# Kernel tuning notes

Measured on AMD Instinct MI355X. Metric: run time of the kernel, lower is better.

Reference implementation:

```python
import jax, jax.numpy as jnp
import numpy as np

B, S, D, H, DFF = 2, 2048, 1024, 16, 4096
DH = D // H
EPS = 1e-12


def _layer_norm(x, g, b):
    mu = jnp.mean(x, axis=-1, keepdims=True)
    var = jnp.mean(jnp.square(x - mu), axis=-1, keepdims=True)
    return (x - mu) * jax.lax.rsqrt(var + EPS) * g + b


def setup_inputs() -> dict:
    key = jax.random.key(0)
    ks = jax.random.split(key, 12)
    s = 0.02
    return {
        "query": jax.random.normal(ks[0], (B, S, D), jnp.float32),
        "key_in": jax.random.normal(ks[1], (B, S, D), jnp.float32),
        "value_in": jax.random.normal(ks[2], (B, S, D), jnp.float32),
        "attention_mask": jnp.zeros((B, 1, 1, S), jnp.float32),
        # weights stored [in, out] (i.e., torch Linear weight transposed)
        "Wq": jax.random.normal(ks[3], (D, D), jnp.float32) * s,
        "bq": jnp.zeros((D,), jnp.float32),
        "Wk": jax.random.normal(ks[4], (D, D), jnp.float32) * s,
        "bk": jnp.zeros((D,), jnp.float32),
        "Wv": jax.random.normal(ks[5], (D, D), jnp.float32) * s,
        "bv": jnp.zeros((D,), jnp.float32),
        "Wo": jax.random.normal(ks[6], (D, D), jnp.float32) * s,
        "bo": jnp.zeros((D,), jnp.float32),
        "ln1_g": jnp.ones((D,), jnp.float32),
        "ln1_b": jnp.zeros((D,), jnp.float32),
        "Wi": jax.random.normal(ks[7], (D, DFF), jnp.float32) * s,
        "bi": jnp.zeros((DFF,), jnp.float32),
        "Wd": jax.random.normal(ks[8], (DFF, D), jnp.float32) * s,
        "bd": jnp.zeros((D,), jnp.float32),
        "ln2_g": jnp.ones((D,), jnp.float32),
        "ln2_b": jnp.zeros((D,), jnp.float32),
    }


def reference(query, key_in, value_in, attention_mask, Wq, bq, Wk, bk, Wv, bv,
              Wo, bo, ln1_g, ln1_b, Wi, bi, Wd, bd, ln2_g, ln2_b):
    # projections -> [B, H, S, DH]
    q = (query @ Wq + bq).reshape(B, S, H, DH).transpose(0, 2, 1, 3)
    k = (key_in @ Wk + bk).reshape(B, S, H, DH).transpose(0, 2, 1, 3)
    v = (value_in @ Wv + bv).reshape(B, S, H, DH).transpose(0, 2, 1, 3)
    # eager attention: full [B,H,S,S] score matrix, as in the source
    scores = jnp.einsum("bhqd,bhkd->bhqk", q, k) / jnp.sqrt(jnp.float32(DH))
    scores = scores + attention_mask
    probs = jax.nn.softmax(scores, axis=-1)  # dropout p=0 -> identity
    ctx = jnp.einsum("bhqk,bhkd->bhqd", probs, v)
    ctx = ctx.transpose(0, 2, 1, 3).reshape(B, S, D)
    attn_out = ctx @ Wo + bo
    attn_out = _layer_norm(attn_out + query, ln1_g, ln1_b)
    inter = jax.nn.gelu(attn_out @ Wi + bi, approximate=False)
    layer_out = inter @ Wd + bd
    return _layer_norm(layer_out + attn_out, ln2_g, ln2_b)
```

## Files before the change

### kernel.cpp

```cpp
#include <hip/hip_runtime.h>
#include <hip/hip_bf16.h>
#include <cmath>

#define B_   2
#define S_   2048
#define D_   1024
#define H_   16
#define DFF_ 4096
#define DH_  64
#define M_   (B_*S_)

typedef __bf16 bfx8 __attribute__((ext_vector_type(8)));
typedef __bf16 bfx4 __attribute__((ext_vector_type(4)));
typedef float  fx4  __attribute__((ext_vector_type(4)));

__device__ __forceinline__ float fast_exp2(float x) {
  float r;
  asm volatile("v_exp_f32 %0, %1" : "=v"(r) : "v"(x));
  return r;
}

__device__ __forceinline__ float fast_erf(float x) {
  float ax = fabsf(x);
  float t  = __builtin_amdgcn_rcpf(fmaf(0.3275911f, ax, 1.0f));
  float p  = fmaf(1.061405429f, t, -1.453152027f);
  p = fmaf(p, t, 1.421413741f);
  p = fmaf(p, t, -0.284496736f);
  p = fmaf(p, t, 0.254829592f);
  p = p * t;
  float e  = fast_exp2(-ax * ax * 1.44269504f);
  float r  = 1.0f - p * e;
  return copysignf(r, x);
}

__device__ __forceinline__ void gload_lds16(const void* g, void* l) {
  __builtin_amdgcn_global_load_lds((__attribute__((address_space(1))) void*)(g),
                                   (__attribute__((address_space(3))) void*)(l),
                                   16, 0, 0);
}

struct CvtArgs { const float* in[3]; __bf16* out[3]; };

__global__ __launch_bounds__(256)
void to_bf16_3_kernel(CvtArgs args, int n) {
  int z = blockIdx.y;
  int i = (blockIdx.x * 256 + threadIdx.x) * 4;
  if (i < n) {
    float4 v = *(const float4*)(args.in[z] + i);
    bfx4 o;
    o[0] = (__bf16)v.x; o[1] = (__bf16)v.y; o[2] = (__bf16)v.z; o[3] = (__bf16)v.w;
    *(bfx4*)(args.out[z] + i) = o;
  }
}

__global__ __launch_bounds__(256)
void scale_mask_kernel(const float* __restrict__ in, float* __restrict__ out, int n) {
  int i = blockIdx.x * 256 + threadIdx.x;
  if (i < n) out[i] = in[i] * 1.44269504f;
}

struct TrArgs { const float* in[6]; __bf16* out[6]; };

__global__ __launch_bounds__(256)
void transpose_all_kernel(TrArgs a) {
  __shared__ float t[32][33];
  int bid = blockIdx.x;
  int wsel, tr, tc, R, C;
  if (bid < 4096) {
    wsel = bid >> 10; int l = bid & 1023;
    tr = l >> 5; tc = l & 31; R = D_; C = D_;
  } else if (bid < 8192) {
    wsel = 4; int l = bid - 4096;
    tr = l >> 7; tc = l & 127; R = D_; C = DFF_;
  } else {
    wsel = 5; int l = bid - 8192;
    tr = l >> 5; tc = l & 31; R = DFF_; C = D_;
  }
  const float* in = a.in[wsel];
  __bf16* out = a.out[wsel];
  int r0 = tr * 32, c0 = tc * 32;
  int tx = threadIdx.x & 31, ty = threadIdx.x >> 5;
#pragma unroll
  for (int j = 0; j < 4; ++j) {
    int r = ty + j * 8;
    t[r][tx] = in[(size_t)(r0 + r) * C + c0 + tx];
  }
  __syncthreads();
#pragma unroll
  for (int j = 0; j < 4; ++j) {
    int c = ty + j * 8;
    out[(size_t)(c0 + c) * R + r0 + tx] = (__bf16)t[tx][c];
  }
}

__global__ __launch_bounds__(256)
void transpose_v_kernel(const __bf16* __restrict__ vb, __bf16* __restrict__ vt) {
  __shared__ __bf16 t[32][33];
  int bh = blockIdx.z;
  int b = bh >> 4, h = bh & 15;
  int s0 = blockIdx.x * 32, d0 = blockIdx.y * 32;
  int tx = threadIdx.x, ty = threadIdx.y;
#pragma unroll
  for (int j = 0; j < 4; ++j) {
    int s = ty + j * 8;
    t[s][tx] = vb[(size_t)((b * S_ + s0 + s) * H_ + h) * DH_ + d0 + tx];
  }
  __syncthreads();
#pragma unroll
  for (int j = 0; j < 4; ++j) {
    int d = ty + j * 8;
    vt[(size_t)(bh * DH_ + d0 + d) * S_ + s0 + tx] = t[tx][d];
  }
}

template<int MODE, int TBN>
__global__ __launch_bounds__(256)
void gemm_kernel(const __bf16* __restrict__ A, const __bf16* __restrict__ Bt,
                 const float* __restrict__ bias, const void* __restrict__ res,
                 void* __restrict__ out, int Ndim, int Kdim) {
  __shared__ alignas(16) __bf16 As[2 * 128 * 64];
  __shared__ alignas(16) __bf16 Bs[2 * TBN * 64];
  const int tid  = threadIdx.x;
  const int lane = tid & 63;
  const int w    = tid >> 6;
  const int wm   = w >> 1, wn = w & 1;
  constexpr int NF = TBN / 32;
  const int m0 = blockIdx.y * 128, n0 = blockIdx.x * TBN;

  fx4 acc[4][NF];
#pragma unroll
  for (int i = 0; i < 4; ++i)
#pragma unroll
    for (int j = 0; j < NF; ++j) acc[i][j] = {0.f, 0.f, 0.f, 0.f};

  const int KT = Kdim / 64;

  auto stage = [&](int kt, int buf) {
    const int kb0 = kt * 64;
#pragma unroll
    for (int i = 0; i < 4; ++i) {
      int o   = tid * 16 + i * 4096;
      int row = o >> 7, cb = o & 127;
      int cbs = cb ^ ((row & 7) << 4);
      gload_lds16((const char*)A + ((size_t)(m0 + row) * Kdim + kb0) * 2 + cbs,
                  (char*)As + buf * 16384 + o);
    }
#pragma unroll
    for (int i = 0; i < NF; ++i) {
      int o   = tid * 16 + i * 4096;
      int row = o >> 7, cb = o & 127;
      int cbs = cb ^ ((row & 7) << 4);
      gload_lds16((const char*)Bt + ((size_t)(n0 + row) * Kdim + kb0) * 2 + cbs,
                  (char*)Bs + buf * (TBN * 128) + o);
    }
  };

  stage(0, 0);
  asm volatile("s_waitcnt vmcnt(0)" ::: "memory");
  __builtin_amdgcn_s_barrier();
  __builtin_amdgcn_sched_barrier(0);

  for (int kt = 0; kt < KT; ++kt) {
    if (kt + 1 < KT) stage(kt + 1, (kt + 1) & 1);
    __builtin_amdgcn_sched_barrier(0);
    if (kt > 0) {
      if (kt + 1 < KT) {
        if constexpr (TBN == 64) asm volatile("s_waitcnt vmcnt(6)" ::: "memory");
        else                     asm volatile("s_waitcnt vmcnt(8)" ::: "memory");
      } else {
        asm volatile("s_waitcnt vmcnt(0)" ::: "memory");
      }
      __builtin_amdgcn_s_barrier();
      __builtin_amdgcn_sched_barrier(0);
    }
    const char* Ab = (const char*)As + (kt & 1) * 16384;
    const char* Bb = (const char*)Bs + (kt & 1) * (TBN * 128);

#pragma unroll
    for (int kk = 0; kk < 2; ++kk) {
      bfx8 afr[4], bfr[NF];
      const int cb = kk * 64 + ((lane >> 4) << 4);
#pragma unroll
      for (int mf = 0; mf < 4; ++mf) {
        int row = wm * 64 + mf * 16 + (lane & 15);
        afr[mf] = *(const bfx8*)(Ab + row * 128 + (cb ^ ((row & 7) << 4)));
      }
#pragma unroll
      for (int nf = 0; nf < NF; ++nf) {
        int row = wn * (TBN / 2) + nf * 16 + (lane & 15);
        bfr[nf] = *(const bfx8*)(Bb + row * 128 + (cb ^ ((row & 7) << 4)));
      }
#pragma unroll
      for (int mf = 0; mf < 4; ++mf)
#pragma unroll
        for (int nf = 0; nf < NF; ++nf)
          acc[mf][nf] = __builtin_amdgcn_mfma_f32_16x16x32_bf16(afr[mf], bfr[nf],
                                                                acc[mf][nf], 0, 0, 0);
    }
    __builtin_amdgcn_s_barrier();
    __builtin_amdgcn_sched_barrier(0);
  }

#pragma unroll
  for (int mf = 0; mf < 4; ++mf) {
#pragma unroll
    for (int nf = 0; nf < NF; ++nf) {
      int col = n0 + wn * (TBN / 2) + nf * 16 + (lane & 15);
      float bvl = bias[col];
#pragma unroll
      for (int r = 0; r < 4; ++r) {
        int rowg = m0 + wm * 64 + mf * 16 + ((lane >> 4) << 2) + r;
        float v = acc[mf][nf][r] + bvl;
        if (MODE == 2) v = 0.5f * v * (1.0f + fast_erf(v * 0.70710678118654752f));
        if (MODE == 4) v += (float)((const __bf16*)res)[(size_t)rowg * Ndim + col];
        if (MODE == 1) ((float*)out)[(size_t)rowg * Ndim + col] = v;
        else           ((__bf16*)out)[(size_t)rowg * Ndim + col] = (__bf16)v;
      }
    }
  }
}

__device__ __forceinline__ void stage_a256(const __bf16* __restrict__ A, int m0,
                                           int Kdim, int tile, int h, char* Asm) {
  char* dst = Asm + (tile & 1) * 32768;
  const int kb0 = tile * 64;
  const int tid = threadIdx.x;
#pragma unroll
  for (int it = 0; it < 2; ++it) {
    int o = tid * 16 + it * 8192;
    int lrow = o >> 7, cb = o & 127;
    int r = (lrow & 63) + h * 64 + ((lrow >> 6) << 7);
    int csrc = cb ^ ((r & 7) << 4);
    gload_lds16((const char*)A + ((size_t)(m0 + r) * Kdim + kb0) * 2 + csrc,
                dst + r * 128 + cb);
  }
}
__device__ __forceinline__ void stage_b256(const __bf16* __restrict__ Bt, int n0,
                                           int Kdim, int tile, int h, char* Bsm) {
  char* dst = Bsm + (tile & 1) * 32768;
  const int kb0 = tile * 64;
  const int tid = threadIdx.x;
#pragma unroll
  for (int it = 0; it < 2; ++it) {
    int o = tid * 16 + it * 8192;
    int lrow = o >> 7, cb = o & 127;
    int r = h * 128 + lrow;
    int csrc = cb ^ ((r & 7) << 4);
    gload_lds16((const char*)Bt + ((size_t)(n0 + r) * Kdim + kb0) * 2 + csrc,
                dst + r * 128 + cb);
  }
}

template<int MODE>
__device__ __forceinline__ void gemm256_body(const __bf16* __restrict__ A,
                                             const __bf16* __restrict__ Bt,
                                             const float* __restrict__ bias,
                                             void* __restrict__ out,
                                             int Ndim, int Kdim, int m0, int n0) {
  extern __shared__ char smem[];
  char* Asm = smem;
  char* Bsm = smem + 65536;
  const int tid  = threadIdx.x;
  const int lane = tid & 63;
  const int w    = tid >> 6;
  const int wm   = w >> 2;
  const int wn   = w & 3;
  const int g    = lane >> 4;
  const int ql   = lane & 15;
  const int KT   = Kdim / 64;

  fx4 acc[8][4];
#pragma unroll
  for (int i = 0; i < 8; ++i)
#pragma unroll
    for (int j = 0; j < 4; ++j) acc[i][j] = {0.f, 0.f, 0.f, 0.f};

  stage_a256(A, m0, Kdim, 0, 0, Asm);
  stage_a256(A, m0, Kdim, 0, 1, Asm);
  stage_b256(Bt, n0, Kdim, 0, 0, Bsm);
  stage_b256(Bt, n0, Kdim, 0, 1, Bsm);
  stage_a256(A, m0, Kdim, 1, 0, Asm);
  asm volatile("s_waitcnt vmcnt(2)" ::: "memory");
  __builtin_amdgcn_s_barrier();
  __builtin_amdgcn_sched_barrier(0);

  for (int t = 0; t < KT; ++t) {
    const char* Ab = Asm + (t & 1) * 32768;
    const char* Bb = Bsm + (t & 1) * 32768;
#pragma unroll
    for (int p = 0; p < 4; ++p) {
      const int ah = p >> 1, kk = p & 1;
      if (p == 0 && t + 1 < KT) stage_a256(A, m0, Kdim, t + 1, 1, Asm);
      if (p == 1 && t + 1 < KT) stage_b256(Bt, n0, Kdim, t + 1, 0, Bsm);
      if (p == 2 && t + 1 < KT) stage_b256(Bt, n0, Kdim, t + 1, 1, Bsm);
      if (p == 3 && t + 2 < KT) stage_a256(A, m0, Kdim, t + 2, 0, Asm);
      __builtin_amdgcn_sched_barrier(0);

      bfx8 af[4], bf[4];
      const int cbv = kk * 64 + g * 16;
#pragma unroll
      for (int j = 0; j < 4; ++j) {
        int arow = wm * 128 + (ah * 4 + j) * 16 + ql;
        af[j] = *(const bfx8*)(Ab + arow * 128 + (cbv ^ ((arow & 7) << 4)));
      }
#pragma unroll
      for (int nf = 0; nf < 4; ++nf) {
        int brow = wn * 64 + nf * 16 + ql;
        bf[nf] = *(const bfx8*)(Bb + brow * 128 + (cbv ^ ((brow & 7) << 4)));
      }
      __builtin_amdgcn_sched_barrier(0);
      __builtin_amdgcn_s_barrier();
      asm volatile("s_waitcnt lgkmcnt(0)" ::: "memory");
      __builtin_amdgcn_sched_barrier(0);
      __builtin_amdgcn_s_setprio(1);
#pragma unroll
      for (int j = 0; j < 4; ++j)
#pragma unroll
        for (int nf = 0; nf < 4; ++nf)
          acc[ah * 4 + j][nf] = __builtin_amdgcn_mfma_f32_16x16x32_bf16(
              af[j], bf[nf], acc[ah * 4 + j][nf], 0, 0, 0);
      __builtin_amdgcn_s_setprio(0);
      __builtin_amdgcn_s_barrier();
      __builtin_amdgcn_sched_barrier(0);
    }
    if (t + 1 < KT) {
      if (t + 2 < KT) asm volatile("s_waitcnt vmcnt(2)" ::: "memory");
      else            asm volatile("s_waitcnt vmcnt(0)" ::: "memory");
      __builtin_amdgcn_s_barrier();
      __builtin_amdgcn_sched_barrier(0);
    }
  }

#pragma unroll
  for (int mf = 0; mf < 8; ++mf) {
#pragma unroll
    for (int nf = 0; nf < 4; ++nf) {
      int col = n0 + wn * 64 + nf * 16 + ql;
      float bvl = bias[col];
#pragma unroll
      for (int r = 0; r < 4; ++r) {
        int rowg = m0 + wm * 128 + mf * 16 + g * 4 + r;
        float v = acc[mf][nf][r] + bvl;
        if (MODE == 2) v = 0.5f * v * (1.0f + fast_erf(v * 0.70710678118654752f));
        if (MODE == 1) ((float*)out)[(size_t)rowg * Ndim + col] = v;
        else          ((__bf16*)out)[(size_t)rowg * Ndim + col] = (__bf16)v;
      }
    }
  }
}

template<int MODE>
__global__ __launch_bounds__(512)
void gemm256_kernel(const __bf16* __restrict__ A, const __bf16* __restrict__ Bt,
                    const float* __restrict__ bias, void* __restrict__ out,
                    int Ndim, int Kdim) {
  gemm256_body<MODE>(A, Bt, bias, out, Ndim, Kdim,
                     blockIdx.y * 256, blockIdx.x * 256);
}

struct QKVArgs {
  const __bf16* A[3]; const __bf16* Bt[3]; const float* bias[3]; __bf16* out[3];
};

__global__ __launch_bounds__(512)
void qkv256_kernel(QKVArgs args, int Ndim, int Kdim) {
  int z = blockIdx.z;
  gemm256_body<0>(args.A[z], args.Bt[z], args.bias[z], (void*)args.out[z],
                  Ndim, Kdim, blockIdx.y * 256, blockIdx.x * 256);
}

__global__ __launch_bounds__(512)
void attn_kernel(const __bf16* __restrict__ Qb, const __bf16* __restrict__ Kb,
                 const __bf16* __restrict__ Vt, const float* __restrict__ mask2,
                 __bf16* __restrict__ ctx) {
  __shared__ alignas(16) __bf16 Ks[3 * 64 * 64];
  __shared__ alignas(16) __bf16 Vs[3 * 64 * 64];
  __shared__ alignas(16) __bf16 Ps[8 * 16 * 64];
  __shared__ alignas(16) float  Ms[2048];

  const int tid  = threadIdx.x;
  const int lane = tid & 63;
  const int w    = tid >> 6;
  const int g    = lane >> 4;
  const int ql   = lane & 15;
  const int bh   = blockIdx.y;
  const int b    = bh >> 4;
  const int h    = bh & 15;
  const int q0   = blockIdx.x * 128;

  const size_t kbase  = ((size_t)(b * S_)) * D_ + h * DH_;
  const size_t vtbase = (size_t)bh * DH_ * S_;
  const int NT = S_ / 64;

  char* Qsm = (char*)Ps;
  const size_t qbase = ((size_t)(b * S_) + q0) * D_ + h * DH_;
#pragma unroll
  for (int i = 0; i < 2; ++i) {
    int o   = tid * 16 + i * 8192;
    int row = o >> 7, cb = o & 127;
    int cbs = cb ^ ((row & 7) << 4);
    gload_lds16((const char*)Qb + (qbase + (size_t)row * D_) * 2 + cbs, Qsm + o);
  }
  {
    int o = tid * 16;
    gload_lds16((const char*)mask2 + (size_t)b * S_ * 4 + o, (char*)Ms + o);
  }
  {
    int o   = tid * 16;
    int row = o >> 7, cb = o & 127;
    int cbs = cb ^ ((row & 7) << 4);
    gload_lds16((const char*)Kb + (kbase + (size_t)row * D_) * 2 + cbs, (char*)Ks + o);
    gload_lds16((const char*)Vt + (vtbase + (size_t)row * S_) * 2 + cbs, (char*)Vs + o);
    gload_lds16((const char*)Kb + (kbase + (size_t)(64 + row) * D_) * 2 + cbs,
                (char*)Ks + 8192 + o);
    gload_lds16((const char*)Vt + (vtbase + (size_t)row * S_ + 64) * 2 + cbs,
                (char*)Vs + 8192 + o);
  }
  asm volatile("s_waitcnt vmcnt(4)" ::: "memory");
  __builtin_amdgcn_s_barrier();
  __builtin_amdgcn_sched_barrier(0);

  bfx8 aq[2];
  {
    int row = w * 16 + ql;
#pragma unroll
    for (int kk = 0; kk < 2; ++kk) {
      int cb = kk * 64 + g * 16;
      aq[kk] = *(const bfx8*)(Qsm + row * 128 + (cb ^ ((row & 7) << 4)));
    }
  }
  __syncthreads();
  asm volatile("s_waitcnt vmcnt(2)" ::: "memory");
  __builtin_amdgcn_s_barrier();
  __builtin_amdgcn_sched_barrier(0);

  float mrun = -1e30f, lrun = 0.f;
  fx4 acc[4];
#pragma unroll
  for (int d = 0; d < 4; ++d) acc[d] = {0.f, 0.f, 0.f, 0.f};

  char* pw = (char*)Ps + w * 2048;
  const float SCL = 0.18033688f;

  for (int t = 0; t < NT; ++t) {
    const int kv0 = t * 64;
    if (t + 2 < NT) {
      int o   = tid * 16;
      int row = o >> 7, cb = o & 127;
      int cbs = cb ^ ((row & 7) << 4);
      int nkv = kv0 + 128;
      int bo  = ((t + 2) % 3) * 8192;
      gload_lds16((const char*)Kb + (kbase + (size_t)(nkv + row) * D_) * 2 + cbs,
                  (char*)Ks + bo + o);
      gload_lds16((const char*)Vt + (vtbase + (size_t)row * S_ + nkv) * 2 + cbs,
                  (char*)Vs + bo + o);
    }
    __builtin_amdgcn_sched_barrier(0);
    if (t > 0) {
      if (t + 2 < NT)      asm volatile("s_waitcnt vmcnt(4)" ::: "memory");
      else if (t + 1 < NT) asm volatile("s_waitcnt vmcnt(2)" ::: "memory");
      else                 asm volatile("s_waitcnt vmcnt(0)" ::: "memory");
      __builtin_amdgcn_s_barrier();
      __builtin_amdgcn_sched_barrier(0);
    }
    const char* Kc = (const char*)Ks + (t % 3) * 8192;
    const char* Vc = (const char*)Vs + (t % 3) * 8192;

    fx4 sc[4];
#pragma unroll
    for (int nf = 0; nf < 4; ++nf) sc[nf] = {0.f, 0.f, 0.f, 0.f};
#pragma unroll
    for (int kk = 0; kk < 2; ++kk) {
      const int cb = kk * 64 + g * 16;
      bfx8 bk[4];
#pragma unroll
      for (int nf = 0; nf < 4; ++nf) {
        int row = nf * 16 + ql;
        bk[nf] = *(const bfx8*)(Kc + row * 128 + (cb ^ ((row & 7) << 4)));
      }
#pragma unroll
      for (int nf = 0; nf < 4; ++nf)
        sc[nf] = __builtin_amdgcn_mfma_f32_16x16x32_bf16(bk[nf], aq[kk], sc[nf], 0, 0, 0);
    }

    float sv[4][4];
#pragma unroll
    for (int nf = 0; nf < 4; ++nf) {
      float4 mk = *(const float4*)((const char*)Ms + (kv0 + nf * 16 + g * 4) * 4);
      sv[nf][0] = sc[nf][0] * SCL + mk.x;
      sv[nf][1] = sc[nf][1] * SCL + mk.y;
      sv[nf][2] = sc[nf][2] * SCL + mk.z;
      sv[nf][3] = sc[nf][3] * SCL + mk.w;
    }
    float t0 = fmaxf(fmaxf(sv[0][0], sv[0][1]), fmaxf(sv[0][2], sv[0][3]));
    float t1 = fmaxf(fmaxf(sv[1][0], sv[1][1]), fmaxf(sv[1][2], sv[1][3]));
    float t2 = fmaxf(fmaxf(sv[2][0], sv[2][1]), fmaxf(sv[2][2], sv[2][3]));
    float t3 = fmaxf(fmaxf(sv[3][0], sv[3][1]), fmaxf(sv[3][2], sv[3][3]));
    float mx = fmaxf(fmaxf(t0, t1), fmaxf(t2, t3));
    mx = fmaxf(mx, __shfl_xor(mx, 16));
    mx = fmaxf(mx, __shfl_xor(mx, 32));

    if (!__all(mx <= mrun + 8.0f)) {
      float mnew  = fmaxf(mrun, mx);
      float alpha = fast_exp2(mrun - mnew);
      lrun *= alpha;
      float af[4];
#pragma unroll
      for (int r = 0; r < 4; ++r) af[r] = __shfl(alpha, g * 4 + r);
#pragma unroll
      for (int d = 0; d < 4; ++d)
#pragma unroll
        for (int r = 0; r < 4; ++r) acc[d][r] *= af[r];
      mrun = mnew;
    }

    float ps[4];
#pragma unroll
    for (int nf = 0; nf < 4; ++nf) {
#pragma unroll
      for (int r = 0; r < 4; ++r) sv[nf][r] = fast_exp2(sv[nf][r] - mrun);
      ps[nf] = (sv[nf][0] + sv[nf][1]) + (sv[nf][2] + sv[nf][3]);
    }
    float rs = (ps[0] + ps[1]) + (ps[2] + ps[3]);
    rs += __shfl_xor(rs, 16);
    rs += __shfl_xor(rs, 32);
    lrun += rs;

#pragma unroll
    for (int nf = 0; nf < 4; ++nf) {
      bfx4 pv;
      pv[0] = (__bf16)sv[nf][0]; pv[1] = (__bf16)sv[nf][1];
      pv[2] = (__bf16)sv[nf][2]; pv[3] = (__bf16)sv[nf][3];
      int c = (nf * 32 + g * 8) ^ ((ql & 7) << 4);
      *(bfx4*)(pw + ql * 128 + c) = pv;
    }

    asm volatile("s_waitcnt lgkmcnt(0)" ::: "memory");
    __builtin_amdgcn_sched_barrier(0);

#pragma unroll
    for (int kk = 0; kk < 2; ++kk) {
      int prow = ql;
      int cb   = kk * 64 + g * 16;
      bfx8 ap  = *(const bfx8*)((const char*)pw + prow * 128 + (cb ^ ((prow & 7) << 4)));
#pragma unroll
      for (int d = 0; d < 4; ++d) {
        int vrow = d * 16 + ql;
        bfx8 bv  = *(const bfx8*)(Vc + vrow * 128 + (cb ^ ((vrow & 7) << 4)));
        acc[d] = __builtin_amdgcn_mfma_f32_16x16x32_bf16(ap, bv, acc[d], 0, 0, 0);
      }
    }

    __builtin_amdgcn_s_barrier();
    __builtin_amdgcn_sched_barrier(0);
  }

  float linv = 1.0f / lrun;
#pragma unroll
  for (int r = 0; r < 4; ++r) {
    float inv = __shfl(linv, g * 4 + r);
    int qrow = q0 + w * 16 + g * 4 + r;
    size_t base = ((size_t)(b * S_) + qrow) * D_ + h * DH_;
#pragma unroll
    for (int d = 0; d < 4; ++d)
      ctx[base + d * 16 + ql] = (__bf16)(acc[d][r] * inv);
  }
}

template<bool WRITE_BF16>
__global__ __launch_bounds__(256)
void ln_kernel(const __bf16* __restrict__ a,
               const float* __restrict__ g, const float* __restrict__ beta,
               float* __restrict__ outf, __bf16* __restrict__ outb) {
  const int row = blockIdx.x;
  const int tid = threadIdx.x;
  const size_t base = (size_t)row * D_;
  bfx4 xa = *(const bfx4*)(a + base + tid * 4);
  float x[4] = {(float)xa[0], (float)xa[1], (float)xa[2], (float)xa[3]};
  float s = x[0] + x[1] + x[2] + x[3];
#pragma unroll
  for (int m = 1; m < 64; m <<= 1) s += __shfl_xor(s, m);
  __shared__ float red[8];
  if ((tid & 63) == 0) red[tid >> 6] = s;
  __syncthreads();
  float mu = (red[0] + red[1] + red[2] + red[3]) * (1.0f / D_);
  float v0 = 0.f;
#pragma unroll
  for (int i = 0; i < 4; ++i) { float d = x[i] - mu; v0 += d * d; }
#pragma unroll
  for (int m = 1; m < 64; m <<= 1) v0 += __shfl_xor(v0, m);
  if ((tid & 63) == 0) red[4 + (tid >> 6)] = v0;
  __syncthreads();
  float var = (red[4] + red[5] + red[6] + red[7]) * (1.0f / D_);
  float rs = rsqrtf(var + 1e-12f);
#pragma unroll
  for (int i = 0; i < 4; ++i) {
    int col = tid * 4 + i;
    x[i] = (x[i] - mu) * rs * g[col] + beta[col];
  }
  if (WRITE_BF16) {
    bfx4 o;
    o[0] = (__bf16)x[0]; o[1] = (__bf16)x[1]; o[2] = (__bf16)x[2]; o[3] = (__bf16)x[3];
    *(bfx4*)(outb + base + tid * 4) = o;
  } else {
    *(float4*)(outf + base + tid * 4) = make_float4(x[0], x[1], x[2], x[3]);
  }
}

extern "C" void kernel_launch(void* const* d_in, const int* in_sizes, int n_in,
                              void* d_out, int out_size, void* d_ws, size_t ws_size,
                              hipStream_t stream) {
  const float* query    = (const float*)d_in[0];
  const float* key_in   = (const float*)d_in[1];
  const float* value_in = (const float*)d_in[2];
  const float* mask     = (const float*)d_in[3];
  const float* Wq = (const float*)d_in[4];  const float* bq = (const float*)d_in[5];
  const float* Wk = (const float*)d_in[6];  const float* bk = (const float*)d_in[7];
  const float* Wv = (const float*)d_in[8];  const float* bv = (const float*)d_in[9];
  const float* Wo = (const float*)d_in[10]; const float* bo = (const float*)d_in[11];
  const float* ln1g = (const float*)d_in[12]; const float* ln1b = (const float*)d_in[13];
  const float* Wi = (const float*)d_in[14]; const float* bi = (const float*)d_in[15];
  const float* Wd = (const float*)d_in[16]; const float* bd = (const float*)d_in[17];
  const float* ln2g = (const float*)d_in[18]; const float* ln2b = (const float*)d_in[19];

  char* ws = (char*)d_ws;
  const size_t MB = 1ull << 20;
  if (ws_size < 112 * MB) return;

  __bf16* xq   = (__bf16*)(ws + 0 * MB);
  __bf16* xk   = (__bf16*)(ws + 8 * MB);
  float*  mask2= (float*)(ws + 8 * MB);
  __bf16* xv   = (__bf16*)(ws + 16 * MB);
  __bf16* x1b  = (__bf16*)(ws + 16 * MB);
  __bf16* qb   = (__bf16*)(ws + 24 * MB);
  __bf16* inter= (__bf16*)(ws + 24 * MB);
  __bf16* kb   = (__bf16*)(ws + 32 * MB);
  __bf16* vb   = (__bf16*)(ws + 40 * MB);
  __bf16* alinb= (__bf16*)(ws + 40 * MB);
  __bf16* vt   = (__bf16*)(ws + 48 * MB);
  __bf16* ctxb = (__bf16*)(ws + 56 * MB);
  __bf16* ffb  = (__bf16*)(ws + 56 * MB);
  __bf16* wqt  = (__bf16*)(ws + 88 * MB);
  __bf16* wkt  = (__bf16*)(ws + 90 * MB);
  __bf16* wvt  = (__bf16*)(ws + 92 * MB);
  __bf16* wot  = (__bf16*)(ws + 94 * MB);
  __bf16* wit  = (__bf16*)(ws + 96 * MB);
  __bf16* wdt  = (__bf16*)(ws + 104 * MB);

  dim3 b256(256);
  dim3 tblk(32, 8);
  const int n1 = M_ * D_;

  CvtArgs ca;
  ca.in[0] = query; ca.in[1] = key_in; ca.in[2] = value_in;
  ca.out[0] = xq;   ca.out[1] = xk;    ca.out[2] = xv;
  to_bf16_3_kernel<<<dim3(n1 / 1024, 3), b256, 0, stream>>>(ca, n1);

  TrArgs ta;
  ta.in[0] = Wq; ta.in[1] = Wk; ta.in[2] = Wv; ta.in[3] = Wo; ta.in[4] = Wi; ta.in[5] = Wd;
  ta.out[0] = wqt; ta.out[1] = wkt; ta.out[2] = wvt; ta.out[3] = wot;
  ta.out[4] = wit; ta.out[5] = wdt;
  transpose_all_kernel<<<dim3(12288), b256, 0, stream>>>(ta);

  QKVArgs qa;
  qa.A[0] = xq;  qa.A[1] = xk;  qa.A[2] = xv;
  qa.Bt[0] = wqt; qa.Bt[1] = wkt; qa.Bt[2] = wvt;
  qa.bias[0] = bq; qa.bias[1] = bk; qa.bias[2] = bv;
  qa.out[0] = qb; qa.out[1] = kb; qa.out[2] = vb;
  qkv256_kernel<<<dim3(D_ / 256, M_ / 256, 3), dim3(512), 131072, stream>>>(qa, D_, D_);

  transpose_v_kernel<<<dim3(S_ / 32, 2, B_ * H_), tblk, 0, stream>>>(vb, vt);

  scale_mask_kernel<<<dim3((B_ * S_ + 255) / 256), b256, 0, stream>>>(mask, mask2, B_ * S_);

  attn_kernel<<<dim3(S_ / 128, B_ * H_), dim3(512), 0, stream>>>(qb, kb, vt, mask2, ctxb);

  gemm_kernel<4, 64><<<dim3(D_ / 64, M_ / 128), b256, 0, stream>>>(ctxb, wot, bo, xq, (void*)alinb, D_, D_);

  ln_kernel<true><<<dim3(M_), b256, 0, stream>>>(alinb, ln1g, ln1b, nullptr, x1b);

  gemm256_kernel<2><<<dim3(DFF_ / 256, M_ / 256), dim3(512), 131072, stream>>>(x1b, wit, bi, (void*)inter, DFF_, D_);

  gemm_kernel<4, 64><<<dim3(D_ / 64, M_ / 128), b256, 0, stream>>>(inter, wdt, bd, x1b, (void*)ffb, D_, DFF_);

  ln_kernel<false><<<dim3(M_), b256, 0, stream>>>(ffb, ln2g, ln2b, (float*)d_out, nullptr);
}
```

Baseline: 257.3 us.

## Merge prep kernels, fold mask scaling into attention, compute row sums via MFMA

Merges the weight-transpose and input bf16-conversion kernels into one launch, and removes the separate mask-scaling kernel by scaling the mask in LDS inside the attention kernel. The softmax row sum is now accumulated with an extra MFMA against a ones vector instead of VALU adds and cross-lane shuffles. s_setprio hints are added around MFMA blocks. These changes cut launch overhead and per-tile VALU/shuffle work, at the cost of one extra MFMA per tile and a denominator summed from bf16-rounded probabilities.

```diff
diff --git a/kernel.cpp b/kernel.cpp
--- a/kernel.cpp
+++ b/kernel.cpp
@@ -39,57 +39,50 @@
                                    16, 0, 0);
 }
 
-struct CvtArgs { const float* in[3]; __bf16* out[3]; };
+struct PrepArgs {
+  const float* win[6]; __bf16* wout[6];
+  const float* cin[3]; __bf16* cout[3];
+};
 
 __global__ __launch_bounds__(256)
-void to_bf16_3_kernel(CvtArgs args, int n) {
-  int z = blockIdx.y;
-  int i = (blockIdx.x * 256 + threadIdx.x) * 4;
-  if (i < n) {
-    float4 v = *(const float4*)(args.in[z] + i);
+void prep_kernel(PrepArgs a) {
+  int bid = blockIdx.x;
+  if (bid < 12288) {
+    __shared__ float t[32][33];
+    int wsel, tr, tc, R, C;
+    if (bid < 4096) {
+      wsel = bid >> 10; int l = bid & 1023;
+      tr = l >> 5; tc = l & 31; R = D_; C = D_;
+    } else if (bid < 8192) {
+      wsel = 4; int l = bid - 4096;
+      tr = l >> 7; tc = l & 127; R = D_; C = DFF_;
+    } else {
+      wsel = 5; int l = bid - 8192;
+      tr = l >> 5; tc = l & 31; R = DFF_; C = D_;
+    }
+    const float* in = a.win[wsel];
+    __bf16* out = a.wout[wsel];
+    int r0 = tr * 32, c0 = tc * 32;
+    int tx = threadIdx.x & 31, ty = threadIdx.x >> 5;
+#pragma unroll
+    for (int j = 0; j < 4; ++j) {
+      int r = ty + j * 8;
+      t[r][tx] = in[(size_t)(r0 + r) * C + c0 + tx];
+    }
+    __syncthreads();
+#pragma unroll
+    for (int j = 0; j < 4; ++j) {
+      int c = ty + j * 8;
+      out[(size_t)(c0 + c) * R + r0 + tx] = (__bf16)t[tx][c];
+    }
+  } else {
+    int l = bid - 12288;
+    int z = l >> 12;
+    int i = ((l & 4095) * 256 + threadIdx.x) * 4;
+    float4 v = *(const float4*)(a.cin[z] + i);
     bfx4 o;
     o[0] = (__bf16)v.x; o[1] = (__bf16)v.y; o[2] = (__bf16)v.z; o[3] = (__bf16)v.w;
-    *(bfx4*)(args.out[z] + i) = o;
-  }
-}
-
-__global__ __launch_bounds__(256)
-void scale_mask_kernel(const float* __restrict__ in, float* __restrict__ out, int n) {
-  int i = blockIdx.x * 256 + threadIdx.x;
-  if (i < n) out[i] = in[i] * 1.44269504f;
-}
-
-struct TrArgs { const float* in[6]; __bf16* out[6]; };
-
-__global__ __launch_bounds__(256)
-void transpose_all_kernel(TrArgs a) {
-  __shared__ float t[32][33];
-  int bid = blockIdx.x;
-  int wsel, tr, tc, R, C;
-  if (bid < 4096) {
-    wsel = bid >> 10; int l = bid & 1023;
-    tr = l >> 5; tc = l & 31; R = D_; C = D_;
-  } else if (bid < 8192) {
-    wsel = 4; int l = bid - 4096;
-    tr = l >> 7; tc = l & 127; R = D_; C = DFF_;
-  } else {
-    wsel = 5; int l = bid - 8192;
-    tr = l >> 5; tc = l & 31; R = DFF_; C = D_;
-  }
-  const float* in = a.in[wsel];
-  __bf16* out = a.out[wsel];
-  int r0 = tr * 32, c0 = tc * 32;
-  int tx = threadIdx.x & 31, ty = threadIdx.x >> 5;
-#pragma unroll
-  for (int j = 0; j < 4; ++j) {
-    int r = ty + j * 8;
-    t[r][tx] = in[(size_t)(r0 + r) * C + c0 + tx];
-  }
-  __syncthreads();
-#pragma unroll
-  for (int j = 0; j < 4; ++j) {
-    int c = ty + j * 8;
-    out[(size_t)(c0 + c) * R + r0 + tx] = (__bf16)t[tx][c];
+    *(bfx4*)(a.cout[z] + i) = o;
   }
 }
 
@@ -371,7 +364,7 @@
 
 __global__ __launch_bounds__(512)
 void attn_kernel(const __bf16* __restrict__ Qb, const __bf16* __restrict__ Kb,
-                 const __bf16* __restrict__ Vt, const float* __restrict__ mask2,
+                 const __bf16* __restrict__ Vt, const float* __restrict__ mask,
                  __bf16* __restrict__ ctx) {
   __shared__ alignas(16) __bf16 Ks[3 * 64 * 64];
   __shared__ alignas(16) __bf16 Vs[3 * 64 * 64];
@@ -403,7 +396,7 @@
   }
   {
     int o = tid * 16;
-    gload_lds16((const char*)mask2 + (size_t)b * S_ * 4 + o, (char*)Ms + o);
+    gload_lds16((const char*)mask + (size_t)b * S_ * 4 + o, (char*)Ms + o);
   }
   {
     int o   = tid * 16;
@@ -420,6 +413,13 @@
   __builtin_amdgcn_s_barrier();
   __builtin_amdgcn_sched_barrier(0);
 
+  {
+    float4 mv = *(float4*)((char*)Ms + tid * 16);
+    mv.x *= 1.44269504f; mv.y *= 1.44269504f;
+    mv.z *= 1.44269504f; mv.w *= 1.44269504f;
+    *(float4*)((char*)Ms + tid * 16) = mv;
+  }
+
   bfx8 aq[2];
   {
     int row = w * 16 + ql;
@@ -434,10 +434,15 @@
   __builtin_amdgcn_s_barrier();
   __builtin_amdgcn_sched_barrier(0);
 
-  float mrun = -1e30f, lrun = 0.f;
+  float mrun = -1e30f;
   fx4 acc[4];
+  fx4 accl = {0.f, 0.f, 0.f, 0.f};
 #pragma unroll
   for (int d = 0; d < 4; ++d) acc[d] = {0.f, 0.f, 0.f, 0.f};
+
+  bfx8 ones;
+#pragma unroll
+  for (int j = 0; j < 8; ++j) ones[j] = (__bf16)1.0f;
 
   char* pw = (char*)Ps + w * 2048;
   const float SCL = 0.18033688f;
@@ -478,9 +483,11 @@
         int row = nf * 16 + ql;
         bk[nf] = *(const bfx8*)(Kc + row * 128 + (cb ^ ((row & 7) << 4)));
       }
+      __builtin_amdgcn_s_setprio(1);
 #pragma unroll
       for (int nf = 0; nf < 4; ++nf)
         sc[nf] = __builtin_amdgcn_mfma_f32_16x16x32_bf16(bk[nf], aq[kk], sc[nf], 0, 0, 0);
+      __builtin_amdgcn_s_setprio(0);
     }
 
     float sv[4][4];
@@ -503,7 +510,6 @@
     if (!__all(mx <= mrun + 8.0f)) {
       float mnew  = fmaxf(mrun, mx);
       float alpha = fast_exp2(mrun - mnew);
-      lrun *= alpha;
       float af[4];
 #pragma unroll
       for (int r = 0; r < 4; ++r) af[r] = __shfl(alpha, g * 4 + r);
@@ -511,20 +517,15 @@
       for (int d = 0; d < 4; ++d)
 #pragma unroll
         for (int r = 0; r < 4; ++r) acc[d][r] *= af[r];
+#pragma unroll
+      for (int r = 0; r < 4; ++r) accl[r] *= af[r];
       mrun = mnew;
     }
 
-    float ps[4];
-#pragma unroll
-    for (int nf = 0; nf < 4; ++nf) {
+#pragma unroll
+    for (int nf = 0; nf < 4; ++nf)
 #pragma unroll
       for (int r = 0; r < 4; ++r) sv[nf][r] = fast_exp2(sv[nf][r] - mrun);
-      ps[nf] = (sv[nf][0] + sv[nf][1]) + (sv[nf][2] + sv[nf][3]);
-    }
-    float rs = (ps[0] + ps[1]) + (ps[2] + ps[3]);
-    rs += __shfl_xor(rs, 16);
-    rs += __shfl_xor(rs, 32);
-    lrun += rs;
 
 #pragma unroll
     for (int nf = 0; nf < 4; ++nf) {
@@ -543,22 +544,24 @@
       int prow = ql;
       int cb   = kk * 64 + g * 16;
       bfx8 ap  = *(const bfx8*)((const char*)pw + prow * 128 + (cb ^ ((prow & 7) << 4)));
+      __builtin_amdgcn_s_setprio(1);
 #pragma unroll
       for (int d = 0; d < 4; ++d) {
         int vrow = d * 16 + ql;
         bfx8 bv  = *(const bfx8*)(Vc + vrow * 128 + (cb ^ ((vrow & 7) << 4)));
         acc[d] = __builtin_amdgcn_mfma_f32_16x16x32_bf16(ap, bv, acc[d], 0, 0, 0);
       }
+      accl = __builtin_amdgcn_mfma_f32_16x16x32_bf16(ap, ones, accl, 0, 0, 0);
+      __builtin_amdgcn_s_setprio(0);
     }
 
     __builtin_amdgcn_s_barrier();
     __builtin_amdgcn_sched_barrier(0);
   }
 
-  float linv = 1.0f / lrun;
 #pragma unroll
   for (int r = 0; r < 4; ++r) {
-    float inv = __shfl(linv, g * 4 + r);
+    float inv = 1.0f / accl[r];
     int qrow = q0 + w * 16 + g * 4 + r;
     size_t base = ((size_t)(b * S_) + qrow) * D_ + h * DH_;
 #pragma unroll
@@ -629,7 +632,6 @@
 
   __bf16* xq   = (__bf16*)(ws + 0 * MB);
   __bf16* xk   = (__bf16*)(ws + 8 * MB);
-  float*  mask2= (float*)(ws + 8 * MB);
   __bf16* xv   = (__bf16*)(ws + 16 * MB);
   __bf16* x1b  = (__bf16*)(ws + 16 * MB);
   __bf16* qb   = (__bf16*)(ws + 24 * MB);
@@ -649,18 +651,15 @@
 
   dim3 b256(256);
   dim3 tblk(32, 8);
-  const int n1 = M_ * D_;
-
-  CvtArgs ca;
-  ca.in[0] = query; ca.in[1] = key_in; ca.in[2] = value_in;
-  ca.out[0] = xq;   ca.out[1] = xk;    ca.out[2] = xv;
-  to_bf16_3_kernel<<<dim3(n1 / 1024, 3), b256, 0, stream>>>(ca, n1);
-
-  TrArgs ta;
-  ta.in[0] = Wq; ta.in[1] = Wk; ta.in[2] = Wv; ta.in[3] = Wo; ta.in[4] = Wi; ta.in[5] = Wd;
-  ta.out[0] = wqt; ta.out[1] = wkt; ta.out[2] = wvt; ta.out[3] = wot;
-  ta.out[4] = wit; ta.out[5] = wdt;
-  transpose_all_kernel<<<dim3(12288), b256, 0, stream>>>(ta);
+
+  PrepArgs pa;
+  pa.win[0] = Wq; pa.win[1] = Wk; pa.win[2] = Wv; pa.win[3] = Wo;
+  pa.win[4] = Wi; pa.win[5] = Wd;
+  pa.wout[0] = wqt; pa.wout[1] = wkt; pa.wout[2] = wvt; pa.wout[3] = wot;
+  pa.wout[4] = wit; pa.wout[5] = wdt;
+  pa.cin[0] = query; pa.cin[1] = key_in; pa.cin[2] = value_in;
+  pa.cout[0] = xq;   pa.cout[1] = xk;    pa.cout[2] = xv;
+  prep_kernel<<<dim3(24576), b256, 0, stream>>>(pa);
 
   QKVArgs qa;
   qa.A[0] = xq;  qa.A[1] = xk;  qa.A[2] = xv;
@@ -671,9 +670,7 @@
 
   transpose_v_kernel<<<dim3(S_ / 32, 2, B_ * H_), tblk, 0, stream>>>(vb, vt);
 
-  scale_mask_kernel<<<dim3((B_ * S_ + 255) / 256), b256, 0, stream>>>(mask, mask2, B_ * S_);
-
-  attn_kernel<<<dim3(S_ / 128, B_ * H_), dim3(512), 0, stream>>>(qb, kb, vt, mask2, ctxb);
+  attn_kernel<<<dim3(S_ / 128, B_ * H_), dim3(512), 0, stream>>>(qb, kb, vt, mask, ctxb);
 
   gemm_kernel<4, 64><<<dim3(D_ / 64, M_ / 128), b256, 0, stream>>>(ctxb, wot, bo, xq, (void*)alinb, D_, D_);
 
```

Result: faster. 250.8 us (-2.5%).
